# Kernel tuning notes

Measured on AMD Instinct MI355X. Metric: run time of the kernel, lower is better.

Reference implementation:

```python
import jax, jax.numpy as jnp
import numpy as np

VOCAB, CTX, EMBED, HEADS = 32000, 2048, 1024, 16


def setup_inputs() -> dict:
    key = jax.random.key(0)
    ks = jax.random.split(key, 10)
    E = EMBED
    s = 0.02
    return {
        "x": jax.random.randint(ks[0], (2, 2048), 0, VOCAB, dtype=jnp.int32),
        "tok_emb": jax.random.normal(ks[1], (VOCAB, E), jnp.float32) * s,
        "pos_emb": jax.random.normal(ks[2], (CTX, E), jnp.float32) * s,
        "qkv_w": jax.random.normal(ks[3], (E, 3 * E), jnp.float32) * s,
        "qkv_b": jnp.zeros((3 * E,), jnp.float32),
        "proj_w": jax.random.normal(ks[4], (E, E), jnp.float32) * s,
        "proj_b": jnp.zeros((E,), jnp.float32),
        "fc_w": jax.random.normal(ks[5], (E, VOCAB), jnp.float32) * s,
        "fc_b": jnp.zeros((VOCAB,), jnp.float32),
    }


def reference(x, tok_emb, pos_emb, qkv_w, qkv_b, proj_w, proj_b, fc_w, fc_b):
    B, T = x.shape
    H = HEADS
    E = tok_emb.shape[1]
    hd = E // H
    h = tok_emb[x] + pos_emb[:T][None, :, :]                      # [B,T,E]
    qkv = h @ qkv_w + qkv_b                                       # [B,T,3E]
    q, k, v = jnp.split(qkv, 3, axis=-1)
    # [B,T,E] -> [B,H,T,hd]
    q = q.reshape(B, T, H, hd).transpose(0, 2, 1, 3)
    k = k.reshape(B, T, H, hd).transpose(0, 2, 1, 3)
    v = v.reshape(B, T, H, hd).transpose(0, 2, 1, 3)
    att = jnp.einsum("bhqd,bhkd->bhqk", q, k) / jnp.sqrt(jnp.float32(hd))
    causal = jnp.tril(jnp.ones((T, T), dtype=bool))
    att = jnp.where(causal[None, None], att, jnp.float32(-jnp.inf))
    att = jax.nn.softmax(att, axis=-1)
    out = jnp.einsum("bhqk,bhkd->bhqd", att, v)                   # [B,H,T,hd]
    out = out.transpose(0, 2, 1, 3).reshape(B, T, E)
    out = out @ proj_w + proj_b
    return out @ fc_w + fc_b                                      # [B,T,VOCAB]
```

## Files before the change

kernel.cpp:

```cpp
#include <hip/hip_runtime.h>

#define BATCH 2
#define T 2048
#define E 1024
#define NH 16
#define HD 64
#define M (BATCH*T)
#define K3 (3*E)
#define VOCAB 32000

typedef __attribute__((ext_vector_type(8))) short s16x8;
typedef __attribute__((ext_vector_type(4))) short s16x4;
typedef __attribute__((ext_vector_type(4))) float f32x4;

__device__ inline unsigned short f2bf(float f) {
  union { float f; unsigned u; } x; x.f = f;
  unsigned r = x.u + 0x7fffu + ((x.u >> 16) & 1u);
  return (unsigned short)(r >> 16);
}

__device__ inline void gload16(const void* g, void* l) {
  __builtin_amdgcn_global_load_lds(
      (const __attribute__((address_space(1))) unsigned int*)g,
      (__attribute__((address_space(3))) unsigned int*)l, 16, 0, 0);
}

__global__ __launch_bounds__(256) void k_embed(const int* __restrict__ x,
    const float* __restrict__ tok, const float* __restrict__ pos,
    unsigned short* __restrict__ hb) {
  int row = blockIdx.x;
  int t = row & (T - 1);
  int tokid = x[row];
  int i = threadIdx.x;
  float4 a = ((const float4*)(tok + (size_t)tokid * E))[i];
  float4 p = ((const float4*)(pos + (size_t)t * E))[i];
  s16x4 o;
  o[0] = (short)f2bf(a.x + p.x); o[1] = (short)f2bf(a.y + p.y);
  o[2] = (short)f2bf(a.z + p.z); o[3] = (short)f2bf(a.w + p.w);
  *(s16x4*)(hb + (size_t)row * E + i * 4) = o;
}

__global__ __launch_bounds__(256) void k_wt(const float* __restrict__ W,
    unsigned short* __restrict__ Wt, int N) {
  __shared__ float tile[64][65];
  int n0 = blockIdx.x * 64, k0 = blockIdx.y * 64;
  int t = threadIdx.x;
  int kl = t >> 2, c = t & 3;
  #pragma unroll
  for (int i = 0; i < 4; i++) {
    float4 v4 = *(const float4*)(W + (size_t)(k0 + kl) * N + n0 + c * 16 + i * 4);
    tile[kl][c * 16 + i * 4 + 0] = v4.x;
    tile[kl][c * 16 + i * 4 + 1] = v4.y;
    tile[kl][c * 16 + i * 4 + 2] = v4.z;
    tile[kl][c * 16 + i * 4 + 3] = v4.w;
  }
  __syncthreads();
  #pragma unroll
  for (int j = 0; j < 2; j++) {
    int idx = t + j * 256;
    int nl = idx >> 3, kq = (idx & 7) * 8;
    s16x8 o;
    #pragma unroll
    for (int i = 0; i < 8; i++) o[i] = (short)f2bf(tile[kq + i][nl]);
    *(s16x8*)(Wt + (size_t)(n0 + nl) * 1024 + k0 + kq) = o;
  }
}

template<int MODE>
__global__ __launch_bounds__(256) void k_bgemm(
    const unsigned short* __restrict__ A, const unsigned short* __restrict__ Bt,
    const float* __restrict__ bias, float* __restrict__ C, int N,
    unsigned short* __restrict__ qo, unsigned short* __restrict__ ko,
    unsigned short* __restrict__ vo, unsigned short* __restrict__ Cb) {
  __shared__ char lds[16384];
  char* As = lds;
  char* Bs = lds + 8192;
  int tid = threadIdx.x;
  int lane = tid & 63;
  int wv = tid >> 6;
  int wm = wv >> 1, wn = wv & 1;
  int n0 = blockIdx.x * 128, m0 = blockIdx.y * 128;
  int fr = lane & 15, fq = lane >> 4;

  f32x4 acc[4][4];
  #pragma unroll
  for (int i = 0; i < 4; i++)
    #pragma unroll
    for (int j = 0; j < 4; j++) acc[i][j] = (f32x4){0.f, 0.f, 0.f, 0.f};

  int p0 = tid * 16, p1 = tid * 16 + 4096;
  int r0 = p0 >> 6, c0 = p0 & 63;
  int r1 = p1 >> 6, c1 = p1 & 63;
  int cs0 = c0 ^ (((r0 >> 1) & 3) << 4);
  int cs1 = c1 ^ (((r1 >> 1) & 3) << 4);
  const char* ga0 = (const char*)(A + (size_t)(m0 + r0) * 1024) + cs0;
  const char* ga1 = (const char*)(A + (size_t)(m0 + r1) * 1024) + cs1;
  const char* gb0 = (const char*)(Bt + (size_t)(n0 + r0) * 1024) + cs0;
  const char* gb1 = (const char*)(Bt + (size_t)(n0 + r1) * 1024) + cs1;

  int aoff[4], boff[4];
  #pragma unroll
  for (int i = 0; i < 4; i++) {
    int ra = wm * 64 + i * 16 + fr;
    aoff[i] = ra * 64 + ((fq * 16) ^ (((ra >> 1) & 3) << 4));
    int rb = wn * 64 + i * 16 + fr;
    boff[i] = rb * 64 + ((fq * 16) ^ (((rb >> 1) & 3) << 4));
  }

  for (int kb = 0; kb < 2048; kb += 64) {
    gload16(ga0 + kb, As + p0);
    gload16(ga1 + kb, As + p1);
    gload16(gb0 + kb, Bs + p0);
    gload16(gb1 + kb, Bs + p1);
    __syncthreads();
    s16x8 af[4], bfr[4];
    #pragma unroll
    for (int i = 0; i < 4; i++) af[i] = *(const s16x8*)(As + aoff[i]);
    #pragma unroll
    for (int i = 0; i < 4; i++) bfr[i] = *(const s16x8*)(Bs + boff[i]);
    #pragma unroll
    for (int mi = 0; mi < 4; mi++)
      #pragma unroll
      for (int ni = 0; ni < 4; ni++)
        acc[mi][ni] = __builtin_amdgcn_mfma_f32_16x16x32_bf16(
            af[mi], bfr[ni], acc[mi][ni], 0, 0, 0);
    __syncthreads();
  }

  if (MODE == 1) {
    #pragma unroll
    for (int mi = 0; mi < 4; mi++) {
      #pragma unroll
      for (int ni = 0; ni < 4; ni++) {
        int n = n0 + wn * 64 + ni * 16 + fr;
        int which = n >> 10;
        int e = n & (E - 1);
        int hh = e >> 6, d = e & 63;
        int mb = m0 + wm * 64 + mi * 16 + fq * 4;
        int b = mb >> 11, tt0 = mb & (T - 1);
        float bv = bias[n];
        if (which == 2) {
          s16x4 pk;
          #pragma unroll
          for (int j = 0; j < 4; j++) pk[j] = (short)f2bf(acc[mi][ni][j] + bv);
          *(s16x4*)(vo + ((size_t)(b * NH + hh) * 64 + d) * T + tt0) = pk;
        } else {
          unsigned short* dst = (which == 0) ? qo : ko;
          #pragma unroll
          for (int j = 0; j < 4; j++)
            dst[((size_t)(b * NH + hh) * T + tt0 + j) * 64 + d] =
                f2bf(acc[mi][ni][j] + bv);
        }
      }
    }
  } else {
    #pragma unroll
    for (int mi = 0; mi < 4; mi++) {
      #pragma unroll
      for (int ni = 0; ni < 4; ni++) {
        #pragma unroll
        for (int j = 0; j < 4; j++) {
          int m = m0 + wm * 64 + mi * 16 + fq * 4 + j;
          int n = n0 + wn * 64 + ni * 16 + fr;
          float val = acc[mi][ni][j] + bias[n];
          if (MODE == 0) C[(size_t)m * N + n] = val;
          else           Cb[(size_t)m * 1024 + n] = f2bf(val);
        }
      }
    }
  }
}

__global__ __launch_bounds__(512, 2) void k_fc(
    const unsigned short* __restrict__ A, const unsigned short* __restrict__ Bt,
    const float* __restrict__ bias, float* __restrict__ C) {
  __shared__ __align__(16) char lds[131072];
  int tid = threadIdx.x, lane = tid & 63, wv = tid >> 6;
  int WM = wv >> 2, WN = wv & 3;
  int fr = lane & 15, fq = lane >> 4;

  int bid = blockIdx.x;
  int wg = (bid & 7) * 250 + (bid >> 3);
  int m0 = (wg & 15) * 256;
  int n0 = (wg >> 4) * 256;

  const char* gA[4]; const char* gB[4]; int lo[4];
  #pragma unroll
  for (int j = 0; j < 4; j++) {
    int i = tid + j * 512;
    int r = i >> 3, c = i & 7;
    int cc = c ^ (r & 7);
    gA[j] = (const char*)A + ((size_t)(m0 + r) * 1024 + cc * 8) * 2;
    gB[j] = (const char*)Bt + ((size_t)(n0 + r) * 1024 + cc * 8) * 2;
    lo[j] = i * 16;
  }

  f32x4 acc[8][4];
  #pragma unroll
  for (int i = 0; i < 8; i++)
    #pragma unroll
    for (int j = 0; j < 4; j++) acc[i][j] = (f32x4){0.f, 0.f, 0.f, 0.f};

  #pragma unroll
  for (int j = 0; j < 4; j++) {
    gload16(gA[j], lds + lo[j]);
    gload16(gB[j], lds + 65536 + lo[j]);
  }
  __syncthreads();

  for (int t = 0; t < 16; t++) {
    int cur = t & 1;
    if (t + 1 < 16) {
      int kb = (t + 1) * 128;
      int nxt = cur ^ 1;
      #pragma unroll
      for (int j = 0; j < 4; j++) {
        gload16(gA[j] + kb, lds + nxt * 32768 + lo[j]);
        gload16(gB[j] + kb, lds + 65536 + nxt * 32768 + lo[j]);
      }
    }
    const char* As = lds + cur * 32768;
    const char* Bs = lds + 65536 + cur * 32768;
    #pragma unroll
    for (int kh = 0; kh < 2; kh++) {
      s16x8 af[8], bf[4];
      #pragma unroll
      for (int mi = 0; mi < 8; mi++) {
        int r = WM * 128 + mi * 16 + fr;
        af[mi] = *(const s16x8*)(As + r * 128 + (((kh * 4 + fq) ^ (r & 7)) << 4));
      }
      #pragma unroll
      for (int ni = 0; ni < 4; ni++) {
        int r = WN * 64 + ni * 16 + fr;
        bf[ni] = *(const s16x8*)(Bs + r * 128 + (((kh * 4 + fq) ^ (r & 7)) << 4));
      }
      __builtin_amdgcn_s_setprio(1);
      #pragma unroll
      for (int mi = 0; mi < 8; mi++)
        #pragma unroll
        for (int ni = 0; ni < 4; ni++)
          acc[mi][ni] = __builtin_amdgcn_mfma_f32_16x16x32_bf16(
              af[mi], bf[ni], acc[mi][ni], 0, 0, 0);
      __builtin_amdgcn_s_setprio(0);
    }
    __syncthreads();
  }

  #pragma unroll
  for (int mi = 0; mi < 8; mi++) {
    #pragma unroll
    for (int ni = 0; ni < 4; ni++) {
      int n = n0 + WN * 64 + ni * 16 + fr;
      float bv = bias[n];
      #pragma unroll
      for (int j = 0; j < 4; j++) {
        int m = m0 + WM * 128 + mi * 16 + fq * 4 + j;
        C[(size_t)m * VOCAB + n] = acc[mi][ni][j] + bv;
      }
    }
  }
}

#define BM 128
#define BN 128
#define BKF 32
#define LDT (BM + 4)
__global__ __launch_bounds__(256) void k_gemm32(
    const float* __restrict__ A, const float* __restrict__ Bw,
    const float* __restrict__ bias, float* __restrict__ C, int N) {
  __shared__ float As[BKF * LDT];
  __shared__ float Bs[BKF * LDT];
  int tid = threadIdx.x;
  int tx = tid & 15, ty = tid >> 4;
  int n0 = blockIdx.x * BN;
  int m0 = blockIdx.y * BM;
  float acc[8][8];
  #pragma unroll
  for (int i = 0; i < 8; i++)
    #pragma unroll
    for (int j = 0; j < 8; j++) acc[i][j] = 0.f;
  for (int k0 = 0; k0 < E; k0 += BKF) {
    #pragma unroll
    for (int i = 0; i < 4; i++) {
      int f = i * 256 + tid;
      int ml = f >> 3, c4 = f & 7;
      float4 va = *(const float4*)(A + (size_t)(m0 + ml) * E + k0 + c4 * 4);
      As[(c4 * 4 + 0) * LDT + ml] = va.x;
      As[(c4 * 4 + 1) * LDT + ml] = va.y;
      As[(c4 * 4 + 2) * LDT + ml] = va.z;
      As[(c4 * 4 + 3) * LDT + ml] = va.w;
    }
    #pragma unroll
    for (int i = 0; i < 4; i++) {
      int f = i * 256 + tid;
      int kk = f >> 5, c4 = f & 31;
      float4 vb = *(const float4*)(Bw + (size_t)(k0 + kk) * N + n0 + c4 * 4);
      *(float4*)(Bs + kk * LDT + c4 * 4) = vb;
    }
    __syncthreads();
    #pragma unroll
    for (int kk = 0; kk < BKF; kk++) {
      const float4* ar = (const float4*)(As + kk * LDT);
      const float4* br = (const float4*)(Bs + kk * LDT);
      float4 a0 = ar[ty * 2], a1 = ar[ty * 2 + 1];
      float4 b0 = br[tx * 2], b1 = br[tx * 2 + 1];
      float av[8] = {a0.x, a0.y, a0.z, a0.w, a1.x, a1.y, a1.z, a1.w};
      float bvv[8] = {b0.x, b0.y, b0.z, b0.w, b1.x, b1.y, b1.z, b1.w};
      #pragma unroll
      for (int i = 0; i < 8; i++)
        #pragma unroll
        for (int j = 0; j < 8; j++)
          acc[i][j] = fmaf(av[i], bvv[j], acc[i][j]);
    }
    __syncthreads();
  }
  int mbase = m0 + ty * 8;
  int nbase = n0 + tx * 8;
  #pragma unroll
  for (int i = 0; i < 8; i++) {
    float* crow = C + (size_t)(mbase + i) * N + nbase;
    #pragma unroll
    for (int j = 0; j < 8; j++) crow[j] = acc[i][j] + bias[nbase + j];
  }
}

__global__ __launch_bounds__(256) void k_attn2(
    const unsigned short* __restrict__ qb, const unsigned short* __restrict__ kb,
    const unsigned short* __restrict__ vtb, unsigned short* __restrict__ o) {
  __shared__ char lds[40960];
  int qt = 15 - (int)blockIdx.x;
  int bh = blockIdx.y;
  int b = bh >> 4, hh = bh & 15;
  int tid = threadIdx.x, lane = tid & 63, wv = tid >> 6;
  int fr = lane & 15, fq = lane >> 4;
  int q0 = qt * 128;
  int qw0 = q0 + wv * 32;
  const char* Kg = (const char*)(kb + (size_t)bh * T * 64);
  const char* Vg = (const char*)(vtb + (size_t)bh * 64 * T);
  char* Pl = lds + 32768 + wv * 2048;

  s16x8 qf[2][2];
  #pragma unroll
  for (int g = 0; g < 2; g++) {
    const unsigned short* Qg = qb + ((size_t)bh * T + qw0 + g * 16) * 64;
    qf[g][0] = *(const s16x8*)(Qg + (size_t)fr * 64 + fq * 8);
    qf[g][1] = *(const s16x8*)(Qg + (size_t)fr * 64 + 32 + fq * 8);
  }

  f32x4 po[2][4];
  float mrow[2][4], lrow[2][4];
  #pragma unroll
  for (int g = 0; g < 2; g++)
    #pragma unroll
    for (int j = 0; j < 4; j++) {
      po[g][j] = (f32x4){0.f, 0.f, 0.f, 0.f};
      mrow[g][j] = -1e30f; lrow[g][j] = 0.f;
    }

  int ntiles = qt * 2 + 2;
  int i0 = tid, i1 = tid + 256;
  int sr0 = i0 >> 3, sc0 = ((i0 & 7) ^ (sr0 & 7)) << 4;
  int sr1 = i1 >> 3, sc1 = ((i1 & 7) ^ (sr1 & 7)) << 4;

  {
    gload16(Kg + (size_t)sr0 * 128 + sc0, lds + i0 * 16);
    gload16(Kg + (size_t)sr1 * 128 + sc1, lds + i1 * 16);
    gload16(Vg + (size_t)sr0 * (T * 2) + sc0, lds + 16384 + i0 * 16);
    gload16(Vg + (size_t)sr1 * (T * 2) + sc1, lds + 16384 + i1 * 16);
  }
  __syncthreads();
  int cur = 0;

  for (int kt = 0; kt < ntiles; kt++) {
    int kv0 = kt * 64;
    if (kt + 1 < ntiles) {
      size_t kvn = (size_t)(kv0 + 64);
      char* kd = lds + (cur ^ 1) * 8192;
      char* vd = lds + 16384 + (cur ^ 1) * 8192;
      gload16(Kg + (kvn + sr0) * 128 + sc0, kd + i0 * 16);
      gload16(Kg + (kvn + sr1) * 128 + sc1, kd + i1 * 16);
      gload16(Vg + (size_t)sr0 * (T * 2) + kvn * 2 + sc0, vd + i0 * 16);
      gload16(Vg + (size_t)sr1 * (T * 2) + kvn * 2 + sc1, vd + i1 * 16);
    }
    const char* Kt = lds + cur * 8192;
    const char* Vt = lds + 16384 + cur * 8192;

    #pragma unroll
    for (int g = 0; g < 2; g++) {
      int qw = qw0 + g * 16;
      f32x4 s[4];
      #pragma unroll
      for (int ni = 0; ni < 4; ni++) {
        s[ni] = (f32x4){0.f, 0.f, 0.f, 0.f};
        int r = ni * 16 + fr;
        s16x8 kf0 = *(const s16x8*)(Kt + r * 128 + ((fq ^ (r & 7)) << 4));
        s16x8 kf1 = *(const s16x8*)(Kt + r * 128 + (((4 + fq) ^ (r & 7)) << 4));
        s[ni] = __builtin_amdgcn_mfma_f32_16x16x32_bf16(qf[g][0], kf0, s[ni], 0, 0, 0);
        s[ni] = __builtin_amdgcn_mfma_f32_16x16x32_bf16(qf[g][1], kf1, s[ni], 0, 0, 0);
      }

      bool needm = (kv0 + 63 > qw);
      #pragma unroll
      for (int jj = 0; jj < 4; jj++) {
        int row = qw + fq * 4 + jj;
        float tm = -1e30f;
        #pragma unroll
        for (int ni = 0; ni < 4; ni++) {
          float val = s[ni][jj] * 0.125f;
          if (needm) { int col = kv0 + ni * 16 + fr; if (col > row) val = -1e30f; }
          s[ni][jj] = val;
          tm = fmaxf(tm, val);
        }
        #pragma unroll
        for (int mk = 1; mk < 16; mk <<= 1) tm = fmaxf(tm, __shfl_xor(tm, mk));
        if (__any(tm > mrow[g][jj] + 8.f)) {
          float nm = fmaxf(mrow[g][jj], tm);
          float corr = __expf(mrow[g][jj] - nm);
          mrow[g][jj] = nm;
          #pragma unroll
          for (int ni = 0; ni < 4; ni++) po[g][ni][jj] *= corr;
          lrow[g][jj] *= corr;
        }
        float mref = mrow[g][jj];
        float rs = 0.f;
        #pragma unroll
        for (int ni = 0; ni < 4; ni++) {
          float pv = __expf(s[ni][jj] - mref);
          s[ni][jj] = pv;
          rs += pv;
        }
        #pragma unroll
        for (int mk = 1; mk < 16; mk <<= 1) rs += __shfl_xor(rs, mk);
        lrow[g][jj] += rs;
      }

      asm volatile("s_waitcnt lgkmcnt(0)" ::: "memory");
      #pragma unroll
      for (int ni = 0; ni < 4; ni++) {
        int col = ni * 16 + fr;
        #pragma unroll
        for (int jj = 0; jj < 4; jj++) {
          int qq = fq * 4 + jj;
          *(unsigned short*)(Pl + qq * 128 + (((col >> 3) ^ (qq & 7)) << 4) +
                             (col & 7) * 2) = f2bf(s[ni][jj]);
        }
      }
      asm volatile("s_waitcnt lgkmcnt(0)" ::: "memory");

      s16x8 pa0 = *(const s16x8*)(Pl + fr * 128 + ((fq ^ (fr & 7)) << 4));
      s16x8 pa1 = *(const s16x8*)(Pl + fr * 128 + (((4 + fq) ^ (fr & 7)) << 4));
      #pragma unroll
      for (int ni = 0; ni < 4; ni++) {
        int r = ni * 16 + fr;
        s16x8 vf0 = *(const s16x8*)(Vt + r * 128 + ((fq ^ (r & 7)) << 4));
        s16x8 vf1 = *(const s16x8*)(Vt + r * 128 + (((4 + fq) ^ (r & 7)) << 4));
        po[g][ni] = __builtin_amdgcn_mfma_f32_16x16x32_bf16(pa0, vf0, po[g][ni], 0, 0, 0);
        po[g][ni] = __builtin_amdgcn_mfma_f32_16x16x32_bf16(pa1, vf1, po[g][ni], 0, 0, 0);
      }
    }
    __syncthreads();
    cur ^= 1;
  }

  #pragma unroll
  for (int g = 0; g < 2; g++)
    #pragma unroll
    for (int jj = 0; jj < 4; jj++) {
      float inv = 1.f / lrow[g][jj];
      int row = qw0 + g * 16 + fq * 4 + jj;
      unsigned short* orow = o + ((size_t)(b * T + row)) * E + hh * 64;
      #pragma unroll
      for (int ni = 0; ni < 4; ni++)
        orow[ni * 16 + fr] = f2bf(po[g][ni][jj] * inv);
    }
}

extern "C" void kernel_launch(void* const* d_in, const int* in_sizes, int n_in,
                              void* d_out, int out_size, void* d_ws, size_t ws_size,
                              hipStream_t stream) {
  const int*   x      = (const int*)d_in[0];
  const float* tok    = (const float*)d_in[1];
  const float* pos    = (const float*)d_in[2];
  const float* qkv_w  = (const float*)d_in[3];
  const float* qkv_b  = (const float*)d_in[4];
  const float* proj_w = (const float*)d_in[5];
  const float* proj_b = (const float*)d_in[6];
  const float* fc_w   = (const float*)d_in[7];
  const float* fc_b   = (const float*)d_in[8];
  float* out = (float*)d_out;
  float* ws  = (float*)d_ws;

  unsigned short* hb      = (unsigned short*)out;
  unsigned short* qkv_wt  = (unsigned short*)(out + 2097152);
  unsigned short* qbuf    = (unsigned short*)(out + 3670016);
  unsigned short* kbuf    = (unsigned short*)(out + 5767168);
  unsigned short* vtbuf   = (unsigned short*)(out + 7864320);
  unsigned short* aob     = (unsigned short*)(out + 9961472);
  unsigned short* proj_wt = (unsigned short*)(out + 12058624);

  const size_t WS_FAST = (size_t)(2097152 + 16384000) * 4;

  k_embed<<<M, 256, 0, stream>>>(x, tok, pos, hb);
  k_wt<<<dim3(K3 / 64, 16), 256, 0, stream>>>(qkv_w, qkv_wt, K3);
  k_bgemm<1><<<dim3(K3 / 128, M / 128), 256, 0, stream>>>(
      hb, qkv_wt, qkv_b, nullptr, K3, qbuf, kbuf, vtbuf, nullptr);
  k_attn2<<<dim3(16, 32), 256, 0, stream>>>(qbuf, kbuf, vtbuf, aob);
  k_wt<<<dim3(E / 64, 16), 256, 0, stream>>>(proj_w, proj_wt, E);

  if (ws_size >= WS_FAST) {
    unsigned short* h2b   = (unsigned short*)ws;
    unsigned short* fc_wt = (unsigned short*)(ws + 2097152);
    k_bgemm<2><<<dim3(E / 128, M / 128), 256, 0, stream>>>(
        aob, proj_wt, proj_b, nullptr, E, nullptr, nullptr, nullptr, h2b);
    k_wt<<<dim3(VOCAB / 64, 16), 256, 0, stream>>>(fc_w, fc_wt, VOCAB);
    k_fc<<<dim3((M / 256) * (VOCAB / 256)), 512, 0, stream>>>(
        h2b, fc_wt, fc_b, out);
  } else {
    float* h2 = ws;
    k_bgemm<0><<<dim3(E / 128, M / 128), 256, 0, stream>>>(
        aob, proj_wt, proj_b, h2, E, nullptr, nullptr, nullptr, nullptr);
    k_gemm32<<<dim3(VOCAB / BN, M / BM), 256, 0, stream>>>(
        h2, fc_w, fc_b, out, VOCAB);
  }
}
```

Baseline: 582.8 us.

## Merge embed and weight-transpose launches; overlap fc weight transpose with attention

```diff
diff --git a/kernel.cpp b/kernel.cpp
--- a/kernel.cpp
+++ b/kernel.cpp
@@ -25,26 +25,9 @@
       (__attribute__((address_space(3))) unsigned int*)l, 16, 0, 0);
 }
 
-__global__ __launch_bounds__(256) void k_embed(const int* __restrict__ x,
-    const float* __restrict__ tok, const float* __restrict__ pos,
-    unsigned short* __restrict__ hb) {
-  int row = blockIdx.x;
-  int t = row & (T - 1);
-  int tokid = x[row];
-  int i = threadIdx.x;
-  float4 a = ((const float4*)(tok + (size_t)tokid * E))[i];
-  float4 p = ((const float4*)(pos + (size_t)t * E))[i];
-  s16x4 o;
-  o[0] = (short)f2bf(a.x + p.x); o[1] = (short)f2bf(a.y + p.y);
-  o[2] = (short)f2bf(a.z + p.z); o[3] = (short)f2bf(a.w + p.w);
-  *(s16x4*)(hb + (size_t)row * E + i * 4) = o;
-}
-
-__global__ __launch_bounds__(256) void k_wt(const float* __restrict__ W,
-    unsigned short* __restrict__ Wt, int N) {
-  __shared__ float tile[64][65];
-  int n0 = blockIdx.x * 64, k0 = blockIdx.y * 64;
-  int t = threadIdx.x;
+__device__ inline void wt_body(const float* __restrict__ W,
+    unsigned short* __restrict__ Wt, int N, int n0, int k0, int t,
+    float (*tile)[65]) {
   int kl = t >> 2, c = t & 3;
   #pragma unroll
   for (int i = 0; i < 4; i++) {
@@ -64,6 +47,34 @@
     for (int i = 0; i < 8; i++) o[i] = (short)f2bf(tile[kq + i][nl]);
     *(s16x8*)(Wt + (size_t)(n0 + nl) * 1024 + k0 + kq) = o;
   }
+}
+
+__global__ __launch_bounds__(256) void k_pre(const int* __restrict__ x,
+    const float* __restrict__ tok, const float* __restrict__ pos,
+    unsigned short* __restrict__ hb,
+    const float* __restrict__ qkvw, unsigned short* __restrict__ qkvwt,
+    const float* __restrict__ projw, unsigned short* __restrict__ projwt) {
+  __shared__ __align__(16) float tile[64][65];
+  int gid = blockIdx.x, t = threadIdx.x;
+  if (gid < 4096) {
+    int row = gid;
+    int tt = row & (T - 1);
+    int tokid = x[row];
+    float4 a = ((const float4*)(tok + (size_t)tokid * E))[t];
+    float4 p = ((const float4*)(pos + (size_t)tt * E))[t];
+    s16x4 o;
+    o[0] = (short)f2bf(a.x + p.x); o[1] = (short)f2bf(a.y + p.y);
+    o[2] = (short)f2bf(a.z + p.z); o[3] = (short)f2bf(a.w + p.w);
+    *(s16x4*)(hb + (size_t)row * E + t * 4) = o;
+    return;
+  }
+  if (gid < 4864) {
+    int idx = gid - 4096;
+    wt_body(qkvw, qkvwt, K3, (idx % 48) * 64, (idx / 48) * 64, t, tile);
+    return;
+  }
+  int idx = gid - 4864;
+  wt_body(projw, projwt, E, (idx % 16) * 64, (idx / 16) * 64, t, tile);
 }
 
 template<int MODE>
@@ -324,14 +335,25 @@
   }
 }
 
-__global__ __launch_bounds__(256) void k_attn2(
+__global__ __launch_bounds__(256) void k_attn_wt(
     const unsigned short* __restrict__ qb, const unsigned short* __restrict__ kb,
-    const unsigned short* __restrict__ vtb, unsigned short* __restrict__ o) {
-  __shared__ char lds[40960];
-  int qt = 15 - (int)blockIdx.x;
-  int bh = blockIdx.y;
+    const unsigned short* __restrict__ vtb, unsigned short* __restrict__ o,
+    const float* __restrict__ fcw, unsigned short* __restrict__ fcwt) {
+  __shared__ __align__(16) char lds[40960];
+  int gid = blockIdx.x;
+  int tid = threadIdx.x;
+
+  if (gid >= 512) {
+    int idx = gid - 512;
+    wt_body(fcw, fcwt, VOCAB, (idx % 500) * 64, (idx / 500) * 64, tid,
+            (float(*)[65])lds);
+    return;
+  }
+
+  int qt = 15 - (gid >> 5);
+  int bh = gid & 31;
   int b = bh >> 4, hh = bh & 15;
-  int tid = threadIdx.x, lane = tid & 63, wv = tid >> 6;
+  int lane = tid & 63, wv = tid >> 6;
   int fr = lane & 15, fq = lane >> 4;
   int q0 = qt * 128;
   int qw0 = q0 + wv * 32;
@@ -500,23 +522,21 @@
 
   const size_t WS_FAST = (size_t)(2097152 + 16384000) * 4;
 
-  k_embed<<<M, 256, 0, stream>>>(x, tok, pos, hb);
-  k_wt<<<dim3(K3 / 64, 16), 256, 0, stream>>>(qkv_w, qkv_wt, K3);
+  k_pre<<<5120, 256, 0, stream>>>(x, tok, pos, hb, qkv_w, qkv_wt, proj_w, proj_wt);
   k_bgemm<1><<<dim3(K3 / 128, M / 128), 256, 0, stream>>>(
       hb, qkv_wt, qkv_b, nullptr, K3, qbuf, kbuf, vtbuf, nullptr);
-  k_attn2<<<dim3(16, 32), 256, 0, stream>>>(qbuf, kbuf, vtbuf, aob);
-  k_wt<<<dim3(E / 64, 16), 256, 0, stream>>>(proj_w, proj_wt, E);
 
   if (ws_size >= WS_FAST) {
     unsigned short* h2b   = (unsigned short*)ws;
     unsigned short* fc_wt = (unsigned short*)(ws + 2097152);
+    k_attn_wt<<<8512, 256, 0, stream>>>(qbuf, kbuf, vtbuf, aob, fc_w, fc_wt);
     k_bgemm<2><<<dim3(E / 128, M / 128), 256, 0, stream>>>(
         aob, proj_wt, proj_b, nullptr, E, nullptr, nullptr, nullptr, h2b);
-    k_wt<<<dim3(VOCAB / 64, 16), 256, 0, stream>>>(fc_w, fc_wt, VOCAB);
     k_fc<<<dim3((M / 256) * (VOCAB / 256)), 512, 0, stream>>>(
         h2b, fc_wt, fc_b, out);
   } else {
     float* h2 = ws;
+    k_attn_wt<<<512, 256, 0, stream>>>(qbuf, kbuf, vtbuf, aob, nullptr, nullptr);
     k_bgemm<0><<<dim3(E / 128, M / 128), 256, 0, stream>>>(
         aob, proj_wt, proj_b, h2, E, nullptr, nullptr, nullptr, nullptr);
     k_gemm32<<<dim3(VOCAB / BN, M / BM), 256, 0, stream>>>(
```

New measurement: 522.2 us. 10.4% less time.
